# Optimization experiments

Measured on AMD Instinct MI355X. Metric: run time of the kernel, lower is better.

The kernel has to match this reference:

```python
import jax, jax.numpy as jnp
import numpy as np
import math

NUM_BLOCKS = 4
LN_EPS = 1e-5

def _layernorm(x, g, b):
    mu = x.mean(-1, keepdims=True)
    var = x.var(-1, keepdims=True)
    return (x - mu) * jax.lax.rsqrt(var + LN_EPS) * g + b

def _pos_encoding(T, E, dtype):
    pos = jnp.arange(T, dtype=jnp.float32)[:, None]
    div = jnp.exp(jnp.arange(0, E, 2, dtype=jnp.float32) * (-math.log(10000.0) / E))
    pe = jnp.zeros((T, E), jnp.float32)
    pe = pe.at[:, 0::2].set(jnp.sin(pos * div))
    pe = pe.at[:, 1::2].set(jnp.cos(pos * div))
    return pe.astype(dtype)

def setup_inputs() -> dict:
    key = jax.random.key(0)
    ks = jax.random.split(key, 4)
    V, E, B, T, C = 50257, 128, 32, 2048, 4
    return {
        "tokens": jax.random.randint(ks[0], (B, T), 0, V),
        "emb": jax.random.normal(ks[1], (V, E), jnp.float32),
        "ln_gamma1": jnp.ones((NUM_BLOCKS, E), jnp.float32),
        "ln_beta1": jnp.zeros((NUM_BLOCKS, E), jnp.float32),
        "ln_gamma2": jnp.ones((NUM_BLOCKS, E), jnp.float32),
        "ln_beta2": jnp.zeros((NUM_BLOCKS, E), jnp.float32),
        "q_weights": jax.random.normal(ks[2], (NUM_BLOCKS, E), jnp.float32),
        "W": jax.random.normal(ks[3], (E, C), jnp.float32) / math.sqrt(E),
        "b": jnp.zeros((C,), jnp.float32),
    }

def reference(tokens, emb, ln_gamma1, ln_beta1, ln_gamma2, ln_beta2, q_weights, W, b):
    # token embedding + sinusoidal PE
    x = emb[tokens]                                  # [B,T,E]
    T, E = x.shape[1], x.shape[2]
    x = x + _pos_encoding(T, E, x.dtype)[None]
    for i in range(NUM_BLOCKS):
        # Closed-form simulation of the quantum circuit:
        #   RX(x_j) on wire j -> CNOT chain (j -> j+1) -> RZ(w_j) -> <Z_j>
        # After RX, E[z_j] = cos(x_j) independently; CNOT chain makes final bit j
        # the XOR of bits 0..j; RZ is diagonal and does not affect <Z>.
        # Hence <Z_j> = prod_{k<=j} cos(x_k) = cumprod(cos(x)) along the wire axis.
        # (q_weights provably have no effect on the output.)
        q = jnp.cumprod(jnp.cos(x), axis=-1)         # [B,T,E]
        x = _layernorm(x + q, ln_gamma1[i], ln_beta1[i])
        x = _layernorm(x + q, ln_gamma2[i], ln_beta2[i])
    x = x.mean(axis=1)                               # mean-pool over time -> [B,E]
    return x @ W + b                                 # [B,num_classes]
```

## Files before the change

kernel.cpp:

```cpp
#include <hip/hip_runtime.h>


#define NBLK 4
#define E_DIM 128
#define T_LEN 2048
#define B_SZ 32
#define C_CLS 4
#define LN_EPS 1e-5f
#define WG_PER_B 64
#define WAVES_PER_WG 4
#define NUM_WG (B_SZ * WG_PER_B)

#define F_ONE 0x3F800000

typedef float v2f __attribute__((ext_vector_type(2)));
typedef float v4f __attribute__((ext_vector_type(4)));

template <int CTRL, int RMASK, int OLDBITS>
__device__ __forceinline__ float dppf(float v) {
    return __int_as_float(__builtin_amdgcn_update_dpp(
        OLDBITS, __float_as_int(v), CTRL, RMASK, 0xF, false));
}

template <int CTRL>
__device__ __forceinline__ float dpp_add(float s) {
    return s + __int_as_float(__builtin_amdgcn_update_dpp(
        0, __float_as_int(s), CTRL, 0xF, 0xF, true));
}

__device__ __forceinline__ float row16_sum(float s) {
    s = dpp_add<0xB1>(s);
    s = dpp_add<0x4E>(s);
    s = dpp_add<0x141>(s);
    s = dpp_add<0x140>(s);
    return s;
}

__device__ __forceinline__ v4f ld4(const float* p) {
    return *reinterpret_cast<const v4f*>(p);
}

__device__ __forceinline__ void ln8v(const v2f* __restrict__ Y,
                                     const v2f* __restrict__ g,
                                     const v2f* __restrict__ be,
                                     v2f* __restrict__ o) {
    v2f sv = (Y[0] + Y[1]) + (Y[2] + Y[3]);
    v2f qv = Y[0] * Y[0];
    qv = __builtin_elementwise_fma(Y[1], Y[1], qv);
    qv = __builtin_elementwise_fma(Y[2], Y[2], qv);
    qv = __builtin_elementwise_fma(Y[3], Y[3], qv);
    const float S  = row16_sum(sv.x + sv.y);
    const float S2 = row16_sum(qv.x + qv.y);
    const float mu  = S * (1.0f / 128.0f);
    const float var = fmaf(S2, 1.0f / 128.0f, -mu * mu);
    const float r   = rsqrtf(var + LN_EPS);
    const v2f muv = {mu, mu};
    const v2f rv  = {r, r};
    #pragma unroll
    for (int j = 0; j < 4; ++j)
        o[j] = __builtin_elementwise_fma((Y[j] - muv) * rv, g[j], be[j]);
}

template <bool ATOMIC>
__global__ __launch_bounds__(256, 4) void qtc_main(
    const int*   __restrict__ tokens,
    const float* __restrict__ emb,
    const float* __restrict__ g1,
    const float* __restrict__ b1,
    const float* __restrict__ g2,
    const float* __restrict__ b2,
    float*       __restrict__ outp)
{
    __shared__ float part[WAVES_PER_WG][4][E_DIM];

    const int tid  = threadIdx.x;
    const int lane = tid & 63;
    const int wave = tid >> 6;
    const int b    = blockIdx.x / WG_PER_B;
    const int wgb  = blockIdx.x % WG_PER_B;
    const int row  = lane >> 4;
    const int sub  = lane & 15;
    const int e0   = sub * 8;
    const int wid  = wgb * WAVES_PER_WG + wave;

    v2f PE[4];
    float dS[4], dC[4];
    {
        const float t0f = (float)(wid * 4 + row);
        #pragma unroll
        for (int j = 0; j < 4; ++j) {
            const float f = __expf(-(float)(e0 + 2 * j) * (9.210340371976184f / 128.0f));
            PE[j] = (v2f){__sinf(t0f * f), __cosf(t0f * f)};
            dS[j] = __sinf(1024.0f * f);
            dC[j] = __cosf(1024.0f * f);
        }
    }

    v2f Sm[4] = {(v2f)0.0f, (v2f)0.0f, (v2f)0.0f, (v2f)0.0f};
    int tix = b * T_LEN + wid * 4 + row;

    #pragma unroll
    for (int it = 0; it < 2; ++it) {
        const int tok = tokens[tix];
        tix += 1024;
        const v4f v0 = ld4(&emb[tok * E_DIM + e0]);
        const v4f v1 = ld4(&emb[tok * E_DIM + e0 + 4]);
        v2f X[4];
        X[0] = v0.xy + PE[0]; X[1] = v0.zw + PE[1];
        X[2] = v1.xy + PE[2]; X[3] = v1.zw + PE[3];
        #pragma unroll
        for (int j = 0; j < 4; ++j) {
            const float s = PE[j].x, c = PE[j].y;
            PE[j] = (v2f){fmaf(s, dC[j],  c * dS[j]),
                          fmaf(c, dC[j], -s * dS[j])};
        }

        #pragma unroll 1
        for (int i = 0; i < NBLK; ++i) {
            const float* gp1 = g1 + i * E_DIM + e0;
            const float* bp1 = b1 + i * E_DIM + e0;
            const float* gp2 = g2 + i * E_DIM + e0;
            const float* bp2 = b2 + i * E_DIM + e0;
            const v4f G1a = ld4(gp1), G1b = ld4(gp1 + 4);
            const v4f B1a = ld4(bp1), B1b = ld4(bp1 + 4);
            const v4f G2a = ld4(gp2), G2b = ld4(gp2 + 4);
            const v4f B2a = ld4(bp2), B2b = ld4(bp2 + 4);
            const v2f g1v[4] = {G1a.xy, G1a.zw, G1b.xy, G1b.zw};
            const v2f b1v[4] = {B1a.xy, B1a.zw, B1b.xy, B1b.zw};
            const v2f g2v[4] = {G2a.xy, G2a.zw, G2b.xy, G2b.zw};
            const v2f b2v[4] = {B2a.xy, B2a.zw, B2b.xy, B2b.zw};

            const float c0 = __cosf(X[0].x), c1 = __cosf(X[0].y);
            const float c2 = __cosf(X[1].x), c3 = __cosf(X[1].y);
            const float c4 = __cosf(X[2].x), c5 = __cosf(X[2].y);
            const float c6 = __cosf(X[3].x), c7 = __cosf(X[3].y);
            const float p23 = c2 * c3, p45 = c4 * c5, p67 = c6 * c7;
            const float P2 = c0 * c1;
            const float P4 = P2 * p23;
            const float P6 = P4 * p45;
            const float P8 = P6 * p67;
            const float P3 = P2 * c2;
            const float P5 = P4 * c4;
            const float P7 = P6 * c6;
            float sc = P8;
            sc *= dppf<0x111, 0xF, F_ONE>(sc);
            sc *= dppf<0x112, 0xF, F_ONE>(sc);
            sc *= dppf<0x114, 0xF, F_ONE>(sc);
            sc *= dppf<0x118, 0xF, F_ONE>(sc);
            const float ex = dppf<0x111, 0xF, F_ONE>(sc);
            const v2f exv = {ex, ex};
            v2f Q[4];
            Q[0] = exv * (v2f){c0, P2};
            Q[1] = exv * (v2f){P3, P4};
            Q[2] = exv * (v2f){P5, P6};
            Q[3] = exv * (v2f){P7, P8};

            v2f Y[4];
            #pragma unroll
            for (int k = 0; k < 4; ++k) Y[k] = X[k] + Q[k];
            ln8v(Y, g1v, b1v, X);
            #pragma unroll
            for (int k = 0; k < 4; ++k) Y[k] = X[k] + Q[k];
            ln8v(Y, g2v, b2v, X);
        }
        #pragma unroll
        for (int k = 0; k < 4; ++k) Sm[k] += X[k];
    }

    const v4f lo = {Sm[0].x, Sm[0].y, Sm[1].x, Sm[1].y};
    const v4f hi = {Sm[2].x, Sm[2].y, Sm[3].x, Sm[3].y};
    *reinterpret_cast<v4f*>(&part[wave][row][e0])     = lo;
    *reinterpret_cast<v4f*>(&part[wave][row][e0 + 4]) = hi;
    __syncthreads();
    if (tid < E_DIM) {
        float s = 0.0f;
        #pragma unroll
        for (int w = 0; w < WAVES_PER_WG; ++w)
            #pragma unroll
            for (int r = 0; r < 4; ++r)
                s += part[w][r][tid];
        if (ATOMIC)
            atomicAdd(&outp[b * E_DIM + tid], s);
        else
            outp[blockIdx.x * E_DIM + tid] = s;
    }
}

__device__ __forceinline__ float wave_sum_tail(float s) {
    s = dpp_add<0xB1>(s);
    s = dpp_add<0x4E>(s);
    s = dpp_add<0x141>(s);
    s = dpp_add<0x140>(s);
    s = s + __int_as_float(__builtin_amdgcn_update_dpp(
        0, __float_as_int(s), 0x142, 0xA, 0xF, true));
    s = s + __int_as_float(__builtin_amdgcn_update_dpp(
        0, __float_as_int(s), 0x143, 0xC, 0xF, true));
    return s;
}

__global__ __launch_bounds__(64) void qtc_final_p(
    const float* __restrict__ part,
    const float* __restrict__ W,
    const float* __restrict__ bias,
    float*       __restrict__ out)
{
    const int b    = blockIdx.x;
    const int lane = threadIdx.x;
    const int e0   = 2 * lane;
    const float* base = part + (size_t)b * WG_PER_B * E_DIM + e0;
    float p0 = 0.0f, p1 = 0.0f;
    #pragma unroll 8
    for (int w = 0; w < WG_PER_B; ++w) {
        const float2 v = *reinterpret_cast<const float2*>(base + w * E_DIM);
        p0 += v.x; p1 += v.y;
    }
    float acc[C_CLS];
    #pragma unroll
    for (int c = 0; c < C_CLS; ++c)
        acc[c] = fmaf(p0, W[e0 * C_CLS + c], p1 * W[(e0 + 1) * C_CLS + c]);
    #pragma unroll
    for (int c = 0; c < C_CLS; ++c)
        acc[c] = wave_sum_tail(acc[c]);
    if (lane == 63) {
        #pragma unroll
        for (int c = 0; c < C_CLS; ++c)
            out[b * C_CLS + c] = fmaf(acc[c], 1.0f / (float)T_LEN, bias[c]);
    }
}

__global__ __launch_bounds__(64) void qtc_final_a(
    const float* __restrict__ pooled,
    const float* __restrict__ W,
    const float* __restrict__ bias,
    float*       __restrict__ out)
{
    const int b    = blockIdx.x;
    const int lane = threadIdx.x;
    const int e0   = 2 * lane;
    const float p0 = pooled[b * E_DIM + e0];
    const float p1 = pooled[b * E_DIM + e0 + 1];
    float acc[C_CLS];
    #pragma unroll
    for (int c = 0; c < C_CLS; ++c)
        acc[c] = fmaf(p0, W[e0 * C_CLS + c], p1 * W[(e0 + 1) * C_CLS + c]);
    #pragma unroll
    for (int c = 0; c < C_CLS; ++c)
        acc[c] = wave_sum_tail(acc[c]);
    if (lane == 63) {
        #pragma unroll
        for (int c = 0; c < C_CLS; ++c)
            out[b * C_CLS + c] = fmaf(acc[c], 1.0f / (float)T_LEN, bias[c]);
    }
}

extern "C" void kernel_launch(void* const* d_in, const int* in_sizes, int n_in,
                              void* d_out, int out_size, void* d_ws, size_t ws_size,
                              hipStream_t stream) {
    const int*   tokens = (const int*)  d_in[0];
    const float* emb    = (const float*)d_in[1];
    const float* g1     = (const float*)d_in[2];
    const float* b1     = (const float*)d_in[3];
    const float* g2     = (const float*)d_in[4];
    const float* b2     = (const float*)d_in[5];
    const float* W      = (const float*)d_in[7];
    const float* bias   = (const float*)d_in[8];
    float* out = (float*)d_out;

    const size_t part_bytes = (size_t)NUM_WG * E_DIM * sizeof(float);
    if (ws_size >= part_bytes) {
        float* part = (float*)d_ws;
        qtc_main<false><<<NUM_WG, 256, 0, stream>>>(tokens, emb, g1, b1, g2, b2, part);
        qtc_final_p<<<B_SZ, 64, 0, stream>>>(part, W, bias, out);
    } else {
        float* pooled = (float*)d_ws;
        hipMemsetAsync(pooled, 0, B_SZ * E_DIM * sizeof(float), stream);
        qtc_main<true><<<NUM_WG, 256, 0, stream>>>(tokens, emb, g1, b1, g2, b2, pooled);
        qtc_final_a<<<B_SZ, 64, 0, stream>>>(pooled, W, bias, out);
    }
}
```

Baseline: 28.95 us.

## Interleave two token rows per thread and hoist LN params into registers

The main kernel now processes both token rows of a thread together, interleaving their cumprod and layernorm chains so independent work can hide DPP and transcendental latency. The block loop is fully unrolled. All gamma/beta vectors are preloaded into registers once instead of being reloaded each block iteration. Positional encodings are computed directly rather than by rotation recurrence. The final reduction kernel uses 256 threads with a shared-memory two-way split to shorten the serial sum over partials. The cost is higher register pressure, since about 128 parameter floats plus two row states stay live, which could reduce occupancy.

```diff
diff --git a/kernel.cpp b/kernel.cpp
--- a/kernel.cpp
+++ b/kernel.cpp
@@ -38,6 +38,33 @@
 
 __device__ __forceinline__ v4f ld4(const float* p) {
     return *reinterpret_cast<const v4f*>(p);
+}
+
+__device__ __forceinline__ void cumq_v(const v2f* __restrict__ X,
+                                       v2f* __restrict__ Q) {
+    const float c0 = __cosf(X[0].x), c1 = __cosf(X[0].y);
+    const float c2 = __cosf(X[1].x), c3 = __cosf(X[1].y);
+    const float c4 = __cosf(X[2].x), c5 = __cosf(X[2].y);
+    const float c6 = __cosf(X[3].x), c7 = __cosf(X[3].y);
+    const float p23 = c2 * c3, p45 = c4 * c5, p67 = c6 * c7;
+    const float P2 = c0 * c1;
+    const float P4 = P2 * p23;
+    const float P6 = P4 * p45;
+    const float P8 = P6 * p67;
+    const float P3 = P2 * c2;
+    const float P5 = P4 * c4;
+    const float P7 = P6 * c6;
+    float sc = P8;
+    sc *= dppf<0x111, 0xF, F_ONE>(sc);
+    sc *= dppf<0x112, 0xF, F_ONE>(sc);
+    sc *= dppf<0x114, 0xF, F_ONE>(sc);
+    sc *= dppf<0x118, 0xF, F_ONE>(sc);
+    const float ex = dppf<0x111, 0xF, F_ONE>(sc);
+    const v2f exv = {ex, ex};
+    Q[0] = exv * (v2f){c0, P2};
+    Q[1] = exv * (v2f){P3, P4};
+    Q[2] = exv * (v2f){P5, P6};
+    Q[3] = exv * (v2f){P7, P8};
 }
 
 __device__ __forceinline__ void ln8v(const v2f* __restrict__ Y,
@@ -83,92 +110,65 @@
     const int e0   = sub * 8;
     const int wid  = wgb * WAVES_PER_WG + wave;
 
-    v2f PE[4];
-    float dS[4], dC[4];
+    v2f G1[NBLK][4], B1[NBLK][4], G2[NBLK][4], B2[NBLK][4];
+    #pragma unroll
+    for (int i = 0; i < NBLK; ++i) {
+        const v4f a1 = ld4(g1 + i * E_DIM + e0), a2 = ld4(g1 + i * E_DIM + e0 + 4);
+        const v4f c1v = ld4(b1 + i * E_DIM + e0), c2v = ld4(b1 + i * E_DIM + e0 + 4);
+        const v4f d1 = ld4(g2 + i * E_DIM + e0), d2 = ld4(g2 + i * E_DIM + e0 + 4);
+        const v4f e1 = ld4(b2 + i * E_DIM + e0), e2 = ld4(b2 + i * E_DIM + e0 + 4);
+        G1[i][0] = a1.xy;  G1[i][1] = a1.zw;  G1[i][2] = a2.xy;  G1[i][3] = a2.zw;
+        B1[i][0] = c1v.xy; B1[i][1] = c1v.zw; B1[i][2] = c2v.xy; B1[i][3] = c2v.zw;
+        G2[i][0] = d1.xy;  G2[i][1] = d1.zw;  G2[i][2] = d2.xy;  G2[i][3] = d2.zw;
+        B2[i][0] = e1.xy;  B2[i][1] = e1.zw;  B2[i][2] = e2.xy;  B2[i][3] = e2.zw;
+    }
+
+    const int   ta  = wid * 4 + row;
+    const int   tix = b * T_LEN + ta;
+    const int   tokA = tokens[tix];
+    const int   tokB = tokens[tix + 1024];
+    const float tfA = (float)ta;
+    const float tfB = (float)(ta + 1024);
+
+    v2f Xa[4], Xb[4];
     {
-        const float t0f = (float)(wid * 4 + row);
+        const v4f a0 = ld4(&emb[tokA * E_DIM + e0]);
+        const v4f a1 = ld4(&emb[tokA * E_DIM + e0 + 4]);
+        const v4f b0 = ld4(&emb[tokB * E_DIM + e0]);
+        const v4f b1v = ld4(&emb[tokB * E_DIM + e0 + 4]);
+        const v2f ea[4] = {a0.xy, a0.zw, a1.xy, a1.zw};
+        const v2f eb[4] = {b0.xy, b0.zw, b1v.xy, b1v.zw};
         #pragma unroll
         for (int j = 0; j < 4; ++j) {
             const float f = __expf(-(float)(e0 + 2 * j) * (9.210340371976184f / 128.0f));
-            PE[j] = (v2f){__sinf(t0f * f), __cosf(t0f * f)};
-            dS[j] = __sinf(1024.0f * f);
-            dC[j] = __cosf(1024.0f * f);
+            Xa[j] = ea[j] + (v2f){__sinf(tfA * f), __cosf(tfA * f)};
+            Xb[j] = eb[j] + (v2f){__sinf(tfB * f), __cosf(tfB * f)};
         }
     }
 
-    v2f Sm[4] = {(v2f)0.0f, (v2f)0.0f, (v2f)0.0f, (v2f)0.0f};
-    int tix = b * T_LEN + wid * 4 + row;
-
-    #pragma unroll
-    for (int it = 0; it < 2; ++it) {
-        const int tok = tokens[tix];
-        tix += 1024;
-        const v4f v0 = ld4(&emb[tok * E_DIM + e0]);
-        const v4f v1 = ld4(&emb[tok * E_DIM + e0 + 4]);
-        v2f X[4];
-        X[0] = v0.xy + PE[0]; X[1] = v0.zw + PE[1];
-        X[2] = v1.xy + PE[2]; X[3] = v1.zw + PE[3];
-        #pragma unroll
-        for (int j = 0; j < 4; ++j) {
-            const float s = PE[j].x, c = PE[j].y;
-            PE[j] = (v2f){fmaf(s, dC[j],  c * dS[j]),
-                          fmaf(c, dC[j], -s * dS[j])};
-        }
-
-        #pragma unroll 1
-        for (int i = 0; i < NBLK; ++i) {
-            const float* gp1 = g1 + i * E_DIM + e0;
-            const float* bp1 = b1 + i * E_DIM + e0;
-            const float* gp2 = g2 + i * E_DIM + e0;
-            const float* bp2 = b2 + i * E_DIM + e0;
-            const v4f G1a = ld4(gp1), G1b = ld4(gp1 + 4);
-            const v4f B1a = ld4(bp1), B1b = ld4(bp1 + 4);
-            const v4f G2a = ld4(gp2), G2b = ld4(gp2 + 4);
-            const v4f B2a = ld4(bp2), B2b = ld4(bp2 + 4);
-            const v2f g1v[4] = {G1a.xy, G1a.zw, G1b.xy, G1b.zw};
-            const v2f b1v[4] = {B1a.xy, B1a.zw, B1b.xy, B1b.zw};
-            const v2f g2v[4] = {G2a.xy, G2a.zw, G2b.xy, G2b.zw};
-            const v2f b2v[4] = {B2a.xy, B2a.zw, B2b.xy, B2b.zw};
-
-            const float c0 = __cosf(X[0].x), c1 = __cosf(X[0].y);
-            const float c2 = __cosf(X[1].x), c3 = __cosf(X[1].y);
-            const float c4 = __cosf(X[2].x), c5 = __cosf(X[2].y);
-            const float c6 = __cosf(X[3].x), c7 = __cosf(X[3].y);
-            const float p23 = c2 * c3, p45 = c4 * c5, p67 = c6 * c7;
-            const float P2 = c0 * c1;
-            const float P4 = P2 * p23;
-            const float P6 = P4 * p45;
-            const float P8 = P6 * p67;
-            const float P3 = P2 * c2;
-            const float P5 = P4 * c4;
-            const float P7 = P6 * c6;
-            float sc = P8;
-            sc *= dppf<0x111, 0xF, F_ONE>(sc);
-            sc *= dppf<0x112, 0xF, F_ONE>(sc);
-            sc *= dppf<0x114, 0xF, F_ONE>(sc);
-            sc *= dppf<0x118, 0xF, F_ONE>(sc);
-            const float ex = dppf<0x111, 0xF, F_ONE>(sc);
-            const v2f exv = {ex, ex};
-            v2f Q[4];
-            Q[0] = exv * (v2f){c0, P2};
-            Q[1] = exv * (v2f){P3, P4};
-            Q[2] = exv * (v2f){P5, P6};
-            Q[3] = exv * (v2f){P7, P8};
-
-            v2f Y[4];
-            #pragma unroll
-            for (int k = 0; k < 4; ++k) Y[k] = X[k] + Q[k];
-            ln8v(Y, g1v, b1v, X);
-            #pragma unroll
-            for (int k = 0; k < 4; ++k) Y[k] = X[k] + Q[k];
-            ln8v(Y, g2v, b2v, X);
-        }
-        #pragma unroll
-        for (int k = 0; k < 4; ++k) Sm[k] += X[k];
-    }
-
-    const v4f lo = {Sm[0].x, Sm[0].y, Sm[1].x, Sm[1].y};
-    const v4f hi = {Sm[2].x, Sm[2].y, Sm[3].x, Sm[3].y};
+    #pragma unroll
+    for (int i = 0; i < NBLK; ++i) {
+        v2f Qa[4], Qb[4], Y[4];
+        cumq_v(Xa, Qa);
+        cumq_v(Xb, Qb);
+        #pragma unroll
+        for (int k = 0; k < 4; ++k) Y[k] = Xa[k] + Qa[k];
+        ln8v(Y, G1[i], B1[i], Xa);
+        #pragma unroll
+        for (int k = 0; k < 4; ++k) Y[k] = Xb[k] + Qb[k];
+        ln8v(Y, G1[i], B1[i], Xb);
+        #pragma unroll
+        for (int k = 0; k < 4; ++k) Y[k] = Xa[k] + Qa[k];
+        ln8v(Y, G2[i], B2[i], Xa);
+        #pragma unroll
+        for (int k = 0; k < 4; ++k) Y[k] = Xb[k] + Qb[k];
+        ln8v(Y, G2[i], B2[i], Xb);
+    }
+
+    const v4f lo = {Xa[0].x + Xb[0].x, Xa[0].y + Xb[0].y,
+                    Xa[1].x + Xb[1].x, Xa[1].y + Xb[1].y};
+    const v4f hi = {Xa[2].x + Xb[2].x, Xa[2].y + Xb[2].y,
+                    Xa[3].x + Xb[3].x, Xa[3].y + Xb[3].y};
     *reinterpret_cast<v4f*>(&part[wave][row][e0])     = lo;
     *reinterpret_cast<v4f*>(&part[wave][row][e0 + 4]) = hi;
     __syncthreads();
@@ -198,33 +198,45 @@
     return s;
 }
 
-__global__ __launch_bounds__(64) void qtc_final_p(
+__global__ __launch_bounds__(256) void qtc_final_p(
     const float* __restrict__ part,
     const float* __restrict__ W,
     const float* __restrict__ bias,
     float*       __restrict__ out)
 {
-    const int b    = blockIdx.x;
-    const int lane = threadIdx.x;
-    const int e0   = 2 * lane;
-    const float* base = part + (size_t)b * WG_PER_B * E_DIM + e0;
-    float p0 = 0.0f, p1 = 0.0f;
+    __shared__ float red[2][E_DIM];
+    __shared__ float pooled[E_DIM];
+    const int b   = blockIdx.x;
+    const int tid = threadIdx.x;
+    const int e   = tid & 127;
+    const int h   = tid >> 7;
+    const float* base = part + (size_t)b * WG_PER_B * E_DIM + e;
+    float s = 0.0f;
     #pragma unroll 8
-    for (int w = 0; w < WG_PER_B; ++w) {
-        const float2 v = *reinterpret_cast<const float2*>(base + w * E_DIM);
-        p0 += v.x; p1 += v.y;
-    }
-    float acc[C_CLS];
-    #pragma unroll
-    for (int c = 0; c < C_CLS; ++c)
-        acc[c] = fmaf(p0, W[e0 * C_CLS + c], p1 * W[(e0 + 1) * C_CLS + c]);
-    #pragma unroll
-    for (int c = 0; c < C_CLS; ++c)
-        acc[c] = wave_sum_tail(acc[c]);
-    if (lane == 63) {
+    for (int w = h * 32; w < h * 32 + 32; ++w)
+        s += base[w * E_DIM];
+    red[h][e] = s;
+    __syncthreads();
+    if (tid < E_DIM)
+        pooled[tid] = red[0][tid] + red[1][tid];
+    __syncthreads();
+    if (tid < 64) {
+        const int lane = tid;
+        const int e0 = 2 * lane;
+        const float p0 = pooled[e0];
+        const float p1 = pooled[e0 + 1];
+        float acc[C_CLS];
         #pragma unroll
         for (int c = 0; c < C_CLS; ++c)
-            out[b * C_CLS + c] = fmaf(acc[c], 1.0f / (float)T_LEN, bias[c]);
+            acc[c] = fmaf(p0, W[e0 * C_CLS + c], p1 * W[(e0 + 1) * C_CLS + c]);
+        #pragma unroll
+        for (int c = 0; c < C_CLS; ++c)
+            acc[c] = wave_sum_tail(acc[c]);
+        if (lane == 63) {
+            #pragma unroll
+            for (int c = 0; c < C_CLS; ++c)
+                out[b * C_CLS + c] = fmaf(acc[c], 1.0f / (float)T_LEN, bias[c]);
+        }
     }
 }
 
@@ -270,7 +282,7 @@
     if (ws_size >= part_bytes) {
         float* part = (float*)d_ws;
         qtc_main<false><<<NUM_WG, 256, 0, stream>>>(tokens, emb, g1, b1, g2, b2, part);
-        qtc_final_p<<<B_SZ, 64, 0, stream>>>(part, W, bias, out);
+        qtc_final_p<<<B_SZ, 256, 0, stream>>>(part, W, bias, out);
     } else {
         float* pooled = (float*)d_ws;
         hipMemsetAsync(pooled, 0, B_SZ * E_DIM * sizeof(float), stream);
```

Measured after the change: 28.26 us (median of 2 runs). 1.02x faster.
